# Kernel optimization log

Hardware: AMD Instinct MI355X
Metric: run time of the kernel (lower is better)

## Reference

```python
import jax, jax.numpy as jnp
import numpy as np

N = 50000   # nodes
E = 800000  # edges (avg degree 16)
G = 64      # graphs in batch

def _lin(k, fi, fo):
    kw, kb = jax.random.split(k)
    s = 1.0 / np.sqrt(fi)
    w = jax.random.uniform(kw, (fi, fo), minval=-s, maxval=s, dtype=jnp.float32)
    b = jax.random.uniform(kb, (fo,), minval=-s, maxval=s, dtype=jnp.float32)
    return w, b

def setup_inputs():
    key = jax.random.key(0)
    ks = jax.random.split(key, 12)
    pos = jax.random.normal(ks[0], (N, 3), dtype=jnp.float32)
    edge_index = jax.random.randint(ks[1], (2, E), 0, N, dtype=jnp.int32)
    batch = jnp.sort(jax.random.randint(ks[2], (N,), 0, G, dtype=jnp.int32))
    w_proj, b_proj = _lin(ks[3], 3, 64)
    # message passing layers: self-weight, neighbor-weight, bias
    ws0, bb0 = _lin(ks[4], 64, 64);  wn0, _ = _lin(jax.random.fold_in(ks[4], 1), 64, 64)
    ws1, bb1 = _lin(ks[5], 64, 64);  wn1, _ = _lin(jax.random.fold_in(ks[5], 1), 64, 64)
    ws2, bb2 = _lin(ks[6], 64, 128); wn2, _ = _lin(jax.random.fold_in(ks[6], 1), 64, 128)
    ws3, bb3 = _lin(ks[7], 256, 256); wn3, _ = _lin(jax.random.fold_in(ks[7], 1), 256, 256)
    # dense head: concat(max, mean) = 512 -> 512 -> 256
    wd1, bd1 = _lin(ks[8], 512, 512)
    wd2, bd2 = _lin(ks[9], 512, 256)
    return {"pos": pos, "edge_index": edge_index, "batch": batch,
            "w_proj": w_proj, "b_proj": b_proj,
            "ws0": ws0, "wn0": wn0, "bb0": bb0,
            "ws1": ws1, "wn1": wn1, "bb1": bb1,
            "ws2": ws2, "wn2": wn2, "bb2": bb2,
            "ws3": ws3, "wn3": wn3, "bb3": bb3,
            "wd1": wd1, "bd1": bd1, "wd2": wd2, "bd2": bd2}

def reference(pos, edge_index, batch, w_proj, b_proj,
              ws0, wn0, bb0, ws1, wn1, bb1, ws2, wn2, bb2, ws3, wn3, bb3,
              wd1, bd1, wd2, bd2):
    src, dst = edge_index[0], edge_index[1]
    x = pos @ w_proj + b_proj  # node projection [N,64]
    # in-degree counts, computed once
    deg = jnp.maximum(
        jax.ops.segment_sum(jnp.ones((E, 1), x.dtype), dst, num_segments=N), 1.0)

    def mp(h, ws, wn, b):
        # mean-aggregate neighbor messages: gather on src, scatter-add on dst
        agg = jax.ops.segment_sum(h[src], dst, num_segments=N) / deg
        return jax.nn.leaky_relu(h @ ws + agg @ wn + b)

    h0 = mp(x, ws0, wn0, bb0)   # [N,64]
    h1 = mp(h0, ws1, wn1, bb1)  # [N,64]
    h2 = mp(h1, ws2, wn2, bb2)  # [N,128]
    nf = mp(jnp.concatenate([h0, h1, h2], axis=-1), ws3, wn3, bb3)  # [N,256]

    # scatter max/mean pooling over graph ids
    gcnt = jnp.maximum(
        jax.ops.segment_sum(jnp.ones((N, 1), nf.dtype), batch, num_segments=G), 1.0)
    x1 = jax.ops.segment_max(nf, batch, num_segments=G)
    x2 = jax.ops.segment_sum(nf, batch, num_segments=G) / gcnt
    g = jnp.concatenate([x1, x2], axis=-1)  # [G,512]

    g = jax.nn.leaky_relu(g @ wd1 + bd1)
    return g @ wd2 + bd2  # [G,256]
```

## Files before the change

kernel.cpp:

```cpp
#include <hip/hip_runtime.h>
#include <math.h>

typedef _Float16 f16x8 __attribute__((ext_vector_type(8)));
typedef unsigned short us8 __attribute__((ext_vector_type(8)));
typedef float f32x4 __attribute__((ext_vector_type(4)));

__device__ inline unsigned short f2h(float f) {
    _Float16 h = (_Float16)f;
    return *(unsigned short*)&h;
}
__device__ inline float h2f(unsigned short u) {
    _Float16 h = *(_Float16*)&u;
    return (float)h;
}

__device__ __forceinline__ size_t pkoff(int row, int col, int KT) {
    return ((size_t)(row >> 4) * (KT >> 5) + (col >> 5)) * 512
         + (size_t)(((col >> 3) & 3) * 128 + ((row & 15) << 3) + (col & 7));
}

#define ECH 4096

__global__ __launch_bounds__(256)
void bucket_hist(const int* __restrict__ edst, int* __restrict__ bcnt, int E, int NB) {
    __shared__ int h[512];
    int tid = threadIdx.x;
    for (int i = tid; i < NB; i += 256) h[i] = 0;
    __syncthreads();
    int c0 = blockIdx.x * ECH, c1 = min(c0 + ECH, E);
    for (int e = c0 + tid; e < c1; e += 256) atomicAdd(&h[edst[e] >> 7], 1);
    __syncthreads();
    for (int i = tid; i < NB; i += 256) if (h[i]) atomicAdd(&bcnt[i], h[i]);
}

__global__ __launch_bounds__(512)
void bucket_scan(const int* __restrict__ bcnt, int* __restrict__ bbase,
                 int* __restrict__ bcur, int* __restrict__ rowstart, int NB, int n) {
    __shared__ int ws[8];
    int tid = threadIdx.x, lane = tid & 63, wid = tid >> 6;
    int v = (tid < NB) ? bcnt[tid] : 0;
    int x = v;
    for (int d = 1; d < 64; d <<= 1) { int y = __shfl_up(x, d); if (lane >= d) x += y; }
    if (lane == 63) ws[wid] = x;
    __syncthreads();
    int off = 0;
    for (int w = 0; w < wid; w++) off += ws[w];
    int excl = x - v + off;
    if (tid < NB) { bbase[tid] = excl; bcur[tid] = excl; }
    if (tid == 0) {
        int tot = 0;
        for (int w = 0; w < 8; w++) tot += ws[w];
        bbase[NB] = tot;
        rowstart[n] = tot;
    }
}

__global__ __launch_bounds__(256)
void bucket_scatter(const int* __restrict__ esrc_in, const int* __restrict__ edst_in,
                    int* __restrict__ bcur, unsigned* __restrict__ bedge, int E, int NB) {
    __shared__ int h[512];
    __shared__ int rb[512];
    int tid = threadIdx.x;
    for (int i = tid; i < NB; i += 256) h[i] = 0;
    __syncthreads();
    int c0 = blockIdx.x * ECH, c1 = min(c0 + ECH, E);
    for (int e = c0 + tid; e < c1; e += 256) atomicAdd(&h[edst_in[e] >> 7], 1);
    __syncthreads();
    for (int i = tid; i < NB; i += 256) {
        rb[i] = h[i] ? atomicAdd(&bcur[i], h[i]) : 0;
        h[i] = 0;
    }
    __syncthreads();
    for (int e = c0 + tid; e < c1; e += 256) {
        int dst = edst_in[e], src = esrc_in[e];
        int b = dst >> 7;
        int o = atomicAdd(&h[b], 1);
        bedge[rb[b] + o] = (unsigned)src | ((unsigned)(dst & 127) << 16);
    }
}

__global__ __launch_bounds__(256)
void node_csr(const unsigned* __restrict__ bedge, const int* __restrict__ bbase,
              int* __restrict__ rowstart, float* __restrict__ degf,
              unsigned short* __restrict__ esrc, int n) {
    __shared__ int cnt[128];
    __shared__ int cur[128];
    __shared__ int ws4[4];
    int b = blockIdx.x, tid = threadIdx.x;
    int lane = tid & 63, wid = tid >> 6;
    int n0 = b << 7;
    int eb0 = bbase[b], eb1 = bbase[b + 1];
    if (tid < 128) cnt[tid] = 0;
    __syncthreads();
    for (int e = eb0 + tid; e < eb1; e += 256) atomicAdd(&cnt[(bedge[e] >> 16) & 127], 1);
    __syncthreads();
    int v = (tid < 128) ? cnt[tid] : 0;
    int x = v;
    for (int d = 1; d < 64; d <<= 1) { int y = __shfl_up(x, d); if (lane >= d) x += y; }
    if (lane == 63) ws4[wid] = x;
    __syncthreads();
    int off = 0;
    for (int w = 0; w < wid; w++) off += ws4[w];
    int excl = x - v + off;
    if (tid < 128 && n0 + tid < n) {
        rowstart[n0 + tid] = eb0 + excl;
        cur[tid] = eb0 + excl;
        degf[n0 + tid] = (float)(v > 0 ? v : 1);
    }
    __syncthreads();
    for (int e = eb0 + tid; e < eb1; e += 256) {
        unsigned u = bedge[e];
        int p = atomicAdd(&cur[(u >> 16) & 127], 1);
        esrc[p] = (unsigned short)(u & 0xffffu);
    }
}

__global__ __launch_bounds__(256)
void prep_k(int* __restrict__ bcnt, float* __restrict__ pmax, float* __restrict__ psum, int G,
            const float* __restrict__ ws0, const float* __restrict__ wn0, unsigned short* __restrict__ WP0,
            const float* __restrict__ ws1, const float* __restrict__ wn1, unsigned short* __restrict__ WP1,
            const float* __restrict__ ws2, const float* __restrict__ wn2, unsigned short* __restrict__ WP2,
            const float* __restrict__ ws3, const float* __restrict__ wn3, unsigned short* __restrict__ WP3) {
    int t = blockIdx.x * 256 + threadIdx.x;
    if (t < 512) bcnt[t] = 0;
    if (t < G * 256) { pmax[t] = -INFINITY; psum[t] = 0.f; }
    if (t < 8192) {
        int k = t >> 6, n = t & 63;
        float v = (k < 64) ? ws0[k * 64 + n] : wn0[(k - 64) * 64 + n];
        WP0[pkoff(n, k, 128)] = f2h(v);
        v = (k < 64) ? ws1[k * 64 + n] : wn1[(k - 64) * 64 + n];
        WP1[pkoff(n, k, 128)] = f2h(v);
    }
    if (t < 16384) {
        int k = t >> 7, n = t & 127;
        float v = (k < 64) ? ws2[k * 128 + n] : wn2[(k - 64) * 128 + n];
        WP2[pkoff(n, k, 128)] = f2h(v);
    }
    if (t < 131072) {
        int k = t >> 8, n = t & 255;
        float v = (k < 256) ? ws3[k * 256 + n] : wn3[(k - 256) * 256 + n];
        WP3[pkoff(n, k, 512)] = f2h(v);
    }
}

__global__ __launch_bounds__(256)
void proj_k(const float* __restrict__ pos, const float* __restrict__ w,
            const float* __restrict__ b, unsigned short* __restrict__ XB0row,
            unsigned short* __restrict__ XB0pk, int n_nodes) {
    int t = blockIdx.x * 256 + threadIdx.x;
    int n = t >> 6, f = t & 63;
    if (n >= n_nodes) return;
    float p0 = pos[n * 3 + 0], p1 = pos[n * 3 + 1], p2 = pos[n * 3 + 2];
    float v = b[f] + p0 * w[f] + p1 * w[64 + f] + p2 * w[128 + f];
    unsigned short h = f2h(v);
    XB0row[(size_t)n * 128 + f] = h;
    XB0pk[pkoff(n, f, 128)] = h;
}

template <int F, int KT>
__global__ __launch_bounds__(256)
void agg_pk(const unsigned short* __restrict__ src, int sstr,
            unsigned short* __restrict__ dpk, int dc,
            const int* __restrict__ rowstart, const unsigned short* __restrict__ esrc,
            const float* __restrict__ degf, int n_nodes) {
    int wave = threadIdx.x >> 6;
    int lane = threadIdx.x & 63;
    int n = blockIdx.x * 4 + wave;
    if (n >= n_nodes) return;
    const int ST = (F == 64) ? 2 : 1;
    int half = (F == 64) ? (lane >> 5) : 0;
    int li   = (F == 64) ? (lane & 31) : lane;
    int e0 = rowstart[n], e1 = rowstart[n + 1];
    float a0 = 0.f, a1 = 0.f;
    int e = e0 + half;
    for (; e + 7 * ST < e1; e += 8 * ST) {
        int s[8];
        unsigned p[8];
        #pragma unroll
        for (int j = 0; j < 8; j++) s[j] = esrc[e + j * ST];
        #pragma unroll
        for (int j = 0; j < 8; j++) p[j] = *(const unsigned*)&src[(size_t)s[j] * sstr + 2 * li];
        #pragma unroll
        for (int j = 0; j < 8; j++) {
            a0 += h2f((unsigned short)(p[j] & 0xffffu));
            a1 += h2f((unsigned short)(p[j] >> 16));
        }
    }
    for (; e + 3 * ST < e1; e += 4 * ST) {
        int s[4];
        unsigned p[4];
        #pragma unroll
        for (int j = 0; j < 4; j++) s[j] = esrc[e + j * ST];
        #pragma unroll
        for (int j = 0; j < 4; j++) p[j] = *(const unsigned*)&src[(size_t)s[j] * sstr + 2 * li];
        #pragma unroll
        for (int j = 0; j < 4; j++) {
            a0 += h2f((unsigned short)(p[j] & 0xffffu));
            a1 += h2f((unsigned short)(p[j] >> 16));
        }
    }
    for (; e < e1; e += ST) {
        int s = esrc[e];
        unsigned p = *(const unsigned*)&src[(size_t)s * sstr + 2 * li];
        a0 += h2f((unsigned short)(p & 0xffffu));
        a1 += h2f((unsigned short)(p >> 16));
    }
    if (F == 64) { a0 += __shfl_xor(a0, 32); a1 += __shfl_xor(a1, 32); }
    float inv = 1.0f / degf[n];
    unsigned out = (unsigned)f2h(a0 * inv) | ((unsigned)f2h(a1 * inv) << 16);
    if (F != 64 || lane < 32) {
        int c = dc + 2 * li;
        *(unsigned*)&dpk[pkoff(n, c, KT)] = out;
    }
}

__device__ inline void atomicMaxFloat(float* addr, float v) {
    if (v >= 0.f) atomicMax((int*)addr, __float_as_int(v));
    else          atomicMin((unsigned int*)addr, __float_as_uint(v));
}

template <int K, int KTA, int MT, int NTB, int POOL>
__global__ __launch_bounds__(256)
void gemm_fr(const unsigned short* __restrict__ Apk, int KA1, int ac1, int ac2,
             const unsigned short* __restrict__ Wpk, const float* __restrict__ bias,
             unsigned short* __restrict__ Drow, int dcol,
             unsigned short* __restrict__ Dpk, int KTD,
             float* __restrict__ pmax, float* __restrict__ psum,
             const int* __restrict__ batch, int M) {
    const int NS = K / 32;
    const int TROW = NTB * 16 + 8;
    const int TSZ = POOL ? 4 : (MT * 16) * TROW;
    __shared__ unsigned short tile_s[4][TSZ];
    int w = threadIdx.x >> 6;
    int lane = threadIdx.x & 63;
    int lm = lane & 15, kb = lane >> 4;
    int rb0 = (blockIdx.x * 4 + w) * MT;
    int nb0 = blockIdx.y * NTB;
    int m0 = rb0 * 16;
    if (m0 >= M) return;
    unsigned short* tile = tile_s[w];

    f32x4 acc[MT][NTB] = {};

    auto loadf = [&](f16x8* A_, f16x8* B_, int s) {
        int kk = s * 32;
        int phys = (kk < KA1) ? (ac1 + kk) : (ac2 + (kk - KA1));
        size_t ak = (size_t)(phys >> 5) * 512 + (size_t)lane * 8;
        #pragma unroll
        for (int mf = 0; mf < MT; mf++)
            A_[mf] = *(const f16x8*)&Apk[(size_t)(rb0 + mf) * (KTA / 32) * 512 + ak];
        #pragma unroll
        for (int nt = 0; nt < NTB; nt++)
            B_[nt] = *(const f16x8*)&Wpk[((size_t)(nb0 + nt) * (K / 32) + s) * 512 + (size_t)lane * 8];
    };
    auto domfma = [&](f16x8* A_, f16x8* B_) {
        #pragma unroll
        for (int nt = 0; nt < NTB; nt++)
            #pragma unroll
            for (int mf = 0; mf < MT; mf++)
                acc[mf][nt] = __builtin_amdgcn_mfma_f32_16x16x32_f16(A_[mf], B_[nt], acc[mf][nt], 0, 0, 0);
    };

    f16x8 aA[MT], bA[NTB], aB[MT], bB[NTB];
    loadf(aA, bA, 0);
    for (int s = 0; s < NS; s += 2) {
        loadf(aB, bB, s + 1);
        domfma(aA, bA);
        if (s + 2 < NS) loadf(aA, bA, s + 2);
        domfma(aB, bB);
    }

    if (!POOL) {
        #pragma unroll
        for (int nt = 0; nt < NTB; nt++) {
            int colL = nt * 16 + lm;
            float bv = bias[nb0 * 16 + colL];
            #pragma unroll
            for (int mf = 0; mf < MT; mf++) {
                #pragma unroll
                for (int r = 0; r < 4; r++) {
                    float v = acc[mf][nt][r] + bv;
                    v = (v > 0.f) ? v : 0.01f * v;
                    unsigned short h = f2h(v);
                    tile[(mf * 16 + kb * 4 + r) * TROW + colL] = h;
                    int gm = m0 + mf * 16 + kb * 4 + r;
                    if (gm < M) Drow[(size_t)gm * 256 + dcol + nb0 * 16 + colL] = h;
                }
            }
        }
        int dkg0 = (dcol + nb0 * 16) >> 5;
        #pragma unroll
        for (int mf = 0; mf < MT; mf++) {
            #pragma unroll
            for (int kg = 0; kg < NTB / 2; kg++) {
                us8 u = *(const us8*)&tile[(mf * 16 + lm) * TROW + kg * 32 + kb * 8];
                *(us8*)&Dpk[((size_t)(rb0 + mf) * (KTD / 32) + dkg0 + kg) * 512 + (size_t)lane * 8] = u;
            }
        }
    } else {
        int grow[MT * 4];
        #pragma unroll
        for (int mf = 0; mf < MT; mf++)
            #pragma unroll
            for (int r = 0; r < 4; r++) {
                int gm = m0 + mf * 16 + kb * 4 + r;
                grow[mf * 4 + r] = batch[gm < M ? gm : (M - 1)];
            }
        int mlast = m0 + MT * 16 - 1;
        bool uni = (batch[m0] == batch[mlast < M ? mlast : (M - 1)]);
        if (uni) {
            int g = grow[0];
            #pragma unroll
            for (int nt = 0; nt < NTB; nt++) {
                int col = (nb0 + nt) * 16 + lm;
                float bv = bias[col];
                float mx = -INFINITY, sm = 0.f;
                #pragma unroll
                for (int mf = 0; mf < MT; mf++) {
                    #pragma unroll
                    for (int r = 0; r < 4; r++) {
                        int gm = m0 + mf * 16 + kb * 4 + r;
                        if (gm >= M) continue;
                        float v = acc[mf][nt][r] + bv;
                        v = (v > 0.f) ? v : 0.01f * v;
                        mx = fmaxf(mx, v); sm += v;
                    }
                }
                mx = fmaxf(mx, __shfl_xor(mx, 16));
                mx = fmaxf(mx, __shfl_xor(mx, 32));
                sm += __shfl_xor(sm, 16);
                sm += __shfl_xor(sm, 32);
                if (kb == 0 && mx > -INFINITY) {
                    atomicMaxFloat(&pmax[g * 256 + col], mx);
                    atomicAdd(&psum[g * 256 + col], sm);
                }
            }
        } else {
            #pragma unroll
            for (int nt = 0; nt < NTB; nt++) {
                int col = (nb0 + nt) * 16 + lm;
                float bv = bias[col];
                int curg = -1; float mx = -INFINITY, sm = 0.f;
                #pragma unroll
                for (int mf = 0; mf < MT; mf++) {
                    #pragma unroll
                    for (int r = 0; r < 4; r++) {
                        int gm = m0 + mf * 16 + kb * 4 + r;
                        if (gm >= M) continue;
                        int g = grow[mf * 4 + r];
                        if (g != curg) {
                            if (curg >= 0) {
                                atomicMaxFloat(&pmax[curg * 256 + col], mx);
                                atomicAdd(&psum[curg * 256 + col], sm);
                            }
                            curg = g; mx = -INFINITY; sm = 0.f;
                        }
                        float v = acc[mf][nt][r] + bv;
                        v = (v > 0.f) ? v : 0.01f * v;
                        mx = fmaxf(mx, v); sm += v;
                    }
                }
                if (curg >= 0) {
                    atomicMaxFloat(&pmax[curg * 256 + col], mx);
                    atomicAdd(&psum[curg * 256 + col], sm);
                }
            }
        }
    }
}

template <int K, int FOUT>
__global__ __launch_bounds__(256)
void gemm_lrelu(const float* __restrict__ A1, int a1s, int a1c, int KA1,
                const float* __restrict__ A2, int a2s, int a2c,
                const float* __restrict__ W1, const float* __restrict__ W2,
                const float* __restrict__ bias,
                float* __restrict__ D, int dstr, int dcol, int M, int doRelu) {
    const int BM = 64, BN = 64, BK = 16;
    __shared__ float As[BK][BM];
    __shared__ float Bs[BK][BN];
    int tid = threadIdx.x;
    int m0 = blockIdx.x * BM;
    int n0 = blockIdx.y * BN;
    int tx = tid & 15;
    int ty = tid >> 4;
    float acc[4][4] = {};
    int mA = tid >> 2;
    int kA = (tid & 3) * 4;
    int kB = tid >> 4;
    int nB = (tid & 15) * 4;
    for (int k0 = 0; k0 < K; k0 += BK) {
        int kk = k0 + kA;
        const float* Ap; int Asr; int Acc;
        if (kk < KA1) { Ap = A1; Asr = a1s; Acc = a1c + kk; }
        else          { Ap = A2; Asr = a2s; Acc = a2c + (kk - KA1); }
        int gm = m0 + mA;
        float4 av;
        if (gm < M) av = *(const float4*)&Ap[(size_t)gm * Asr + Acc];
        else        av = float4{0.f, 0.f, 0.f, 0.f};
        As[kA + 0][mA] = av.x; As[kA + 1][mA] = av.y;
        As[kA + 2][mA] = av.z; As[kA + 3][mA] = av.w;
        int kw = k0 + kB;
        const float* Wp; int kwl;
        if (kw < K / 2) { Wp = W1; kwl = kw; } else { Wp = W2; kwl = kw - K / 2; }
        float4 bv = *(const float4*)&Wp[(size_t)kwl * FOUT + n0 + nB];
        *(float4*)&Bs[kB][nB] = bv;
        __syncthreads();
        #pragma unroll
        for (int k = 0; k < BK; k++) {
            float a[4], b[4];
            *(float4*)a = *(const float4*)&As[k][ty * 4];
            *(float4*)b = *(const float4*)&Bs[k][tx * 4];
            #pragma unroll
            for (int i = 0; i < 4; i++)
                #pragma unroll
                for (int j = 0; j < 4; j++)
                    acc[i][j] += a[i] * b[j];
        }
        __syncthreads();
    }
    #pragma unroll
    for (int i = 0; i < 4; i++) {
        int gm = m0 + ty * 4 + i;
        if (gm >= M) continue;
        #pragma unroll
        for (int j = 0; j < 4; j++) {
            int gn = n0 + tx * 4 + j;
            float v = acc[i][j] + bias[gn];
            if (doRelu) v = (v > 0.f) ? v : 0.01f * v;
            D[(size_t)gm * dstr + dcol + gn] = v;
        }
    }
}

__global__ __launch_bounds__(256)
void pool_final(const float* __restrict__ pmax, const float* __restrict__ psum,
                const int* __restrict__ batch, float* __restrict__ pooled,
                int G, int n_nodes) {
    int t = blockIdx.x * 256 + threadIdx.x;
    if (t >= G * 256) return;
    int g = t >> 8, f = t & 255;
    int lo = 0, hi = n_nodes;
    while (lo < hi) { int mid = (lo + hi) >> 1; if (batch[mid] < g) lo = mid + 1; else hi = mid; }
    int start = lo;
    lo = start; hi = n_nodes;
    while (lo < hi) { int mid = (lo + hi) >> 1; if (batch[mid] < g + 1) lo = mid + 1; else hi = mid; }
    int end = lo;
    int c = end - start;
    float mx = pmax[t];
    if (c == 0) mx = 0.f;
    pooled[g * 512 + f] = mx;
    pooled[g * 512 + 256 + f] = psum[t] / (float)(c > 0 ? c : 1);
}

extern "C" void kernel_launch(void* const* d_in, const int* in_sizes, int n_in,
                              void* d_out, int out_size, void* d_ws, size_t ws_size,
                              hipStream_t stream) {
    const float* pos   = (const float*)d_in[0];
    const int*   eidx  = (const int*)d_in[1];
    const int*   batch = (const int*)d_in[2];
    const float* w_proj = (const float*)d_in[3];
    const float* b_proj = (const float*)d_in[4];
    const float* ws0 = (const float*)d_in[5];  const float* wn0 = (const float*)d_in[6];  const float* bb0 = (const float*)d_in[7];
    const float* ws1 = (const float*)d_in[8];  const float* wn1 = (const float*)d_in[9];  const float* bb1 = (const float*)d_in[10];
    const float* ws2 = (const float*)d_in[11]; const float* wn2 = (const float*)d_in[12]; const float* bb2 = (const float*)d_in[13];
    const float* ws3 = (const float*)d_in[14]; const float* wn3 = (const float*)d_in[15]; const float* bb3 = (const float*)d_in[16];
    const float* wd1 = (const float*)d_in[17]; const float* bd1 = (const float*)d_in[18];
    const float* wd2 = (const float*)d_in[19]; const float* bd2 = (const float*)d_in[20];

    int N = in_sizes[0] / 3;
    int E = in_sizes[1] / 2;
    int G = out_size / 256;
    const int* esrc_in = eidx;
    const int* edst_in = eidx + E;

    int gbx1 = (N + 63) / 64;
    int gbx2 = (N + 127) / 128;
    int NRB = gbx1 * 4 + 8;
    int NB  = (N + 127) >> 7;

    char* base = (char*)d_ws;
    size_t off = 0;
    auto alloc = [&](size_t bytes) -> void* {
        void* p = base + off;
        off = (off + bytes + 255) & ~(size_t)255;
        return p;
    };
    int*   rowstart = (int*)alloc((size_t)(N + 1) * 4);
    float* degf     = (float*)alloc((size_t)N * 4);
    int*   bcnt     = (int*)alloc((size_t)512 * 4);
    int*   bbase    = (int*)alloc((size_t)513 * 4);
    int*   bcur     = (int*)alloc((size_t)512 * 4);
    unsigned* bedge = (unsigned*)alloc((size_t)E * 4);
    unsigned short* esrc = (unsigned short*)alloc((size_t)E * 2);
    unsigned short* XB0row = (unsigned short*)alloc((size_t)N * 128 * 2);
    unsigned short* XB0pk  = (unsigned short*)alloc((size_t)NRB * 16 * 128 * 2);
    unsigned short* XBrow  = (unsigned short*)alloc((size_t)N * 256 * 2);
    unsigned short* XBpk   = (unsigned short*)alloc((size_t)NRB * 16 * 512 * 2);
    float* pooled   = (float*)alloc((size_t)G * 512 * 4);
    float* hid      = (float*)alloc((size_t)G * 512 * 4);
    float* pmax     = (float*)alloc((size_t)G * 256 * 4);
    float* psum     = (float*)alloc((size_t)G * 256 * 4);
    unsigned short* WP0 = (unsigned short*)alloc((size_t)64 * 128 * 2);
    unsigned short* WP1 = (unsigned short*)alloc((size_t)64 * 128 * 2);
    unsigned short* WP2 = (unsigned short*)alloc((size_t)128 * 128 * 2);
    unsigned short* WP3 = (unsigned short*)alloc((size_t)256 * 512 * 2);

    prep_k<<<512, 256, 0, stream>>>(bcnt, pmax, psum, G,
                                    ws0, wn0, WP0, ws1, wn1, WP1,
                                    ws2, wn2, WP2, ws3, wn3, WP3);

    int eb = (E + ECH - 1) / ECH;
    bucket_hist<<<eb, 256, 0, stream>>>(edst_in, bcnt, E, NB);
    bucket_scan<<<1, 512, 0, stream>>>(bcnt, bbase, bcur, rowstart, NB, N);
    bucket_scatter<<<eb, 256, 0, stream>>>(esrc_in, edst_in, bcur, bedge, E, NB);
    node_csr<<<NB, 256, 0, stream>>>(bedge, bbase, rowstart, degf, esrc, N);

    proj_k<<<(N * 64 + 255) / 256, 256, 0, stream>>>(pos, w_proj, b_proj, XB0row, XB0pk, N);

    int ab = (N + 3) / 4;

    agg_pk<64, 128><<<ab, 256, 0, stream>>>(XB0row, 128, XB0pk, 64, rowstart, esrc, degf, N);
    gemm_fr<128, 128, 1, 4, 0><<<dim3(gbx1, 1), 256, 0, stream>>>(
        XB0pk, 128, 0, 0, WP0, bb0, XBrow, 0, XBpk, 512, nullptr, nullptr, nullptr, N);

    agg_pk<64, 512><<<ab, 256, 0, stream>>>(XBrow, 256, XBpk, 256, rowstart, esrc, degf, N);
    gemm_fr<128, 512, 1, 4, 0><<<dim3(gbx1, 1), 256, 0, stream>>>(
        XBpk, 64, 0, 256, WP1, bb1, XBrow, 64, XBpk, 512, nullptr, nullptr, nullptr, N);

    agg_pk<64, 512><<<ab, 256, 0, stream>>>(XBrow + 64, 256, XBpk, 320, rowstart, esrc, degf, N);
    gemm_fr<128, 512, 1, 4, 0><<<dim3(gbx1, 2), 256, 0, stream>>>(
        XBpk, 64, 64, 320, WP2, bb2, XBrow, 128, XBpk, 512, nullptr, nullptr, nullptr, N);

    agg_pk<128, 512><<<ab, 256, 0, stream>>>(XBrow + 128, 256, XBpk, 384, rowstart, esrc, degf, N);
    gemm_fr<512, 512, 2, 4, 1><<<dim3(gbx2, 4), 256, 0, stream>>>(
        XBpk, 512, 0, 0, WP3, bb3, nullptr, 0, nullptr, 512, pmax, psum, batch, N);
    pool_final<<<(G * 256 + 255) / 256, 256, 0, stream>>>(pmax, psum, batch, pooled, G, N);

    gemm_lrelu<512, 512><<<dim3((G + 63) / 64, 8), 256, 0, stream>>>(
        pooled, 512, 0, 512, pooled, 512, 0, wd1, wd1 + 256 * 512, bd1, hid, 512, 0, G, 1);
    gemm_lrelu<512, 256><<<dim3((G + 63) / 64, 4), 256, 0, stream>>>(
        hid, 512, 0, 512, hid, 512, 0, wd2, wd2 + 256 * 256, bd2, (float*)d_out, 256, 0, G, 0);
}
```

Baseline: 303.7 us.

## Fold input projection into layer 0 and aggregate 3-D positions instead of features

Because the projection is linear, layer 0 is rewritten algebraically. The projection weights are premultiplied into the self and neighbour weights, and the neighbour mean is taken over 3-component fp16 positions rather than 64-wide features. This removes the projection kernel, the 64-wide gather for layer 0 and its GEMM, replacing them with one small fused kernel. The layer-3 GEMM launch also changes its tile parameter (4 to 8) and grid (4 to 2 in y). Layer 0 now uses fp16-rounded positions, a different rounding path, and prep_k grows to cover 4N threads.

```diff
diff --git a/kernel.cpp b/kernel.cpp
--- a/kernel.cpp
+++ b/kernel.cpp
@@ -117,18 +117,19 @@
 
 __global__ __launch_bounds__(256)
 void prep_k(int* __restrict__ bcnt, float* __restrict__ pmax, float* __restrict__ psum, int G,
-            const float* __restrict__ ws0, const float* __restrict__ wn0, unsigned short* __restrict__ WP0,
             const float* __restrict__ ws1, const float* __restrict__ wn1, unsigned short* __restrict__ WP1,
             const float* __restrict__ ws2, const float* __restrict__ wn2, unsigned short* __restrict__ WP2,
-            const float* __restrict__ ws3, const float* __restrict__ wn3, unsigned short* __restrict__ WP3) {
+            const float* __restrict__ ws3, const float* __restrict__ wn3, unsigned short* __restrict__ WP3,
+            const float* __restrict__ wp, const float* __restrict__ bp,
+            const float* __restrict__ ws0, const float* __restrict__ wn0, const float* __restrict__ bb0,
+            float* __restrict__ W0c, float* __restrict__ b0c,
+            const float* __restrict__ pos, unsigned short* __restrict__ pos16, int N) {
     int t = blockIdx.x * 256 + threadIdx.x;
     if (t < 512) bcnt[t] = 0;
     if (t < G * 256) { pmax[t] = -INFINITY; psum[t] = 0.f; }
     if (t < 8192) {
         int k = t >> 6, n = t & 63;
-        float v = (k < 64) ? ws0[k * 64 + n] : wn0[(k - 64) * 64 + n];
-        WP0[pkoff(n, k, 128)] = f2h(v);
-        v = (k < 64) ? ws1[k * 64 + n] : wn1[(k - 64) * 64 + n];
+        float v = (k < 64) ? ws1[k * 64 + n] : wn1[(k - 64) * 64 + n];
         WP1[pkoff(n, k, 128)] = f2h(v);
     }
     if (t < 16384) {
@@ -141,20 +142,59 @@
         float v = (k < 256) ? ws3[k * 256 + n] : wn3[(k - 256) * 256 + n];
         WP3[pkoff(n, k, 512)] = f2h(v);
     }
-}
-
-__global__ __launch_bounds__(256)
-void proj_k(const float* __restrict__ pos, const float* __restrict__ w,
-            const float* __restrict__ b, unsigned short* __restrict__ XB0row,
-            unsigned short* __restrict__ XB0pk, int n_nodes) {
-    int t = blockIdx.x * 256 + threadIdx.x;
-    int n = t >> 6, f = t & 63;
+    if (t < 384) {
+        int j = t / 64, f = t & 63;
+        const float* W = (j < 3) ? ws0 : wn0;
+        int jj = (j < 3) ? j : j - 3;
+        float acc = 0.f;
+        for (int c = 0; c < 64; c++) acc += wp[jj * 64 + c] * W[c * 64 + f];
+        W0c[j * 64 + f] = acc;
+    }
+    if (t < 64) {
+        float acc = bb0[t];
+        for (int c = 0; c < 64; c++) acc += bp[c] * (ws0[c * 64 + t] + wn0[c * 64 + t]);
+        b0c[t] = acc;
+    }
+    if (t < 4 * N) {
+        int n = t >> 2, j = t & 3;
+        pos16[t] = (j < 3) ? f2h(pos[n * 3 + j]) : 0;
+    }
+}
+
+__global__ __launch_bounds__(256)
+void l0_k(const float* __restrict__ pos, const unsigned short* __restrict__ pos16,
+          const float* __restrict__ W0c, const float* __restrict__ b0c,
+          const int* __restrict__ rowstart, const unsigned short* __restrict__ esrc,
+          const float* __restrict__ degf,
+          unsigned short* __restrict__ XBrow, unsigned short* __restrict__ XBpk, int n_nodes) {
+    int wave = threadIdx.x >> 6, lane = threadIdx.x & 63;
+    int n = blockIdx.x * 4 + wave;
     if (n >= n_nodes) return;
-    float p0 = pos[n * 3 + 0], p1 = pos[n * 3 + 1], p2 = pos[n * 3 + 2];
-    float v = b[f] + p0 * w[f] + p1 * w[64 + f] + p2 * w[128 + f];
+    int e0 = rowstart[n], e1 = rowstart[n + 1];
+    float ax = 0.f, ay = 0.f, az = 0.f;
+    for (int e = e0 + lane; e < e1; e += 64) {
+        int s = esrc[e];
+        uint2 q = *(const uint2*)&pos16[(size_t)s * 4];
+        ax += h2f((unsigned short)(q.x & 0xffffu));
+        ay += h2f((unsigned short)(q.x >> 16));
+        az += h2f((unsigned short)(q.y & 0xffffu));
+    }
+    #pragma unroll
+    for (int d = 32; d; d >>= 1) {
+        ax += __shfl_xor(ax, d);
+        ay += __shfl_xor(ay, d);
+        az += __shfl_xor(az, d);
+    }
+    float inv = 1.0f / degf[n];
+    ax *= inv; ay *= inv; az *= inv;
+    float px = pos[n * 3 + 0], py = pos[n * 3 + 1], pz = pos[n * 3 + 2];
+    int f = lane;
+    float v = b0c[f] + px * W0c[f] + py * W0c[64 + f] + pz * W0c[128 + f]
+            + ax * W0c[192 + f] + ay * W0c[256 + f] + az * W0c[320 + f];
+    v = (v > 0.f) ? v : 0.01f * v;
     unsigned short h = f2h(v);
-    XB0row[(size_t)n * 128 + f] = h;
-    XB0pk[pkoff(n, f, 128)] = h;
+    XBrow[(size_t)n * 256 + f] = h;
+    XBpk[pkoff(n, f, 512)] = h;
 }
 
 template <int F, int KT>
@@ -493,22 +533,24 @@
     int*   bcur     = (int*)alloc((size_t)512 * 4);
     unsigned* bedge = (unsigned*)alloc((size_t)E * 4);
     unsigned short* esrc = (unsigned short*)alloc((size_t)E * 2);
-    unsigned short* XB0row = (unsigned short*)alloc((size_t)N * 128 * 2);
-    unsigned short* XB0pk  = (unsigned short*)alloc((size_t)NRB * 16 * 128 * 2);
+    unsigned short* pos16 = (unsigned short*)alloc((size_t)N * 4 * 2);
+    float* W0c      = (float*)alloc((size_t)6 * 64 * 4);
+    float* b0c      = (float*)alloc((size_t)64 * 4);
     unsigned short* XBrow  = (unsigned short*)alloc((size_t)N * 256 * 2);
     unsigned short* XBpk   = (unsigned short*)alloc((size_t)NRB * 16 * 512 * 2);
     float* pooled   = (float*)alloc((size_t)G * 512 * 4);
     float* hid      = (float*)alloc((size_t)G * 512 * 4);
     float* pmax     = (float*)alloc((size_t)G * 256 * 4);
     float* psum     = (float*)alloc((size_t)G * 256 * 4);
-    unsigned short* WP0 = (unsigned short*)alloc((size_t)64 * 128 * 2);
     unsigned short* WP1 = (unsigned short*)alloc((size_t)64 * 128 * 2);
     unsigned short* WP2 = (unsigned short*)alloc((size_t)128 * 128 * 2);
     unsigned short* WP3 = (unsigned short*)alloc((size_t)256 * 512 * 2);
 
-    prep_k<<<512, 256, 0, stream>>>(bcnt, pmax, psum, G,
-                                    ws0, wn0, WP0, ws1, wn1, WP1,
-                                    ws2, wn2, WP2, ws3, wn3, WP3);
+    int prep_threads = 4 * N > 131072 ? 4 * N : 131072;
+    prep_k<<<(prep_threads + 255) / 256, 256, 0, stream>>>(
+        bcnt, pmax, psum, G,
+        ws1, wn1, WP1, ws2, wn2, WP2, ws3, wn3, WP3,
+        w_proj, b_proj, ws0, wn0, bb0, W0c, b0c, pos, pos16, N);
 
     int eb = (E + ECH - 1) / ECH;
     bucket_hist<<<eb, 256, 0, stream>>>(edst_in, bcnt, E, NB);
@@ -516,13 +558,9 @@
     bucket_scatter<<<eb, 256, 0, stream>>>(esrc_in, edst_in, bcur, bedge, E, NB);
     node_csr<<<NB, 256, 0, stream>>>(bedge, bbase, rowstart, degf, esrc, N);
 
-    proj_k<<<(N * 64 + 255) / 256, 256, 0, stream>>>(pos, w_proj, b_proj, XB0row, XB0pk, N);
-
     int ab = (N + 3) / 4;
 
-    agg_pk<64, 128><<<ab, 256, 0, stream>>>(XB0row, 128, XB0pk, 64, rowstart, esrc, degf, N);
-    gemm_fr<128, 128, 1, 4, 0><<<dim3(gbx1, 1), 256, 0, stream>>>(
-        XB0pk, 128, 0, 0, WP0, bb0, XBrow, 0, XBpk, 512, nullptr, nullptr, nullptr, N);
+    l0_k<<<ab, 256, 0, stream>>>(pos, pos16, W0c, b0c, rowstart, esrc, degf, XBrow, XBpk, N);
 
     agg_pk<64, 512><<<ab, 256, 0, stream>>>(XBrow, 256, XBpk, 256, rowstart, esrc, degf, N);
     gemm_fr<128, 512, 1, 4, 0><<<dim3(gbx1, 1), 256, 0, stream>>>(
@@ -533,7 +571,7 @@
         XBpk, 64, 64, 320, WP2, bb2, XBrow, 128, XBpk, 512, nullptr, nullptr, nullptr, N);
 
     agg_pk<128, 512><<<ab, 256, 0, stream>>>(XBrow + 128, 256, XBpk, 384, rowstart, esrc, degf, N);
-    gemm_fr<512, 512, 2, 4, 1><<<dim3(gbx2, 4), 256, 0, stream>>>(
+    gemm_fr<512, 512, 2, 8, 1><<<dim3(gbx2, 2), 256, 0, stream>>>(
         XBpk, 512, 0, 0, WP3, bb3, nullptr, 0, nullptr, 512, pmax, psum, batch, N);
     pool_final<<<(G * 256 + 255) / 256, 256, 0, stream>>>(pmax, psum, batch, pooled, G, N);
 
```

After: 281.6 us (median of 2 runs). -7.3%, faster.
